# Kernel optimization log

Measured on AMD Instinct MI355X. Metric: run time of the kernel, lower is better.

Reference implementation:

```python
import math
import jax, jax.numpy as jnp
import numpy as np

GROUPS = 8

def setup_inputs() -> dict:
    key = jax.random.key(0)
    ks = jax.random.split(key, 6)
    N, H, W, C = 8, 128, 128, 512
    s = 1.0 / math.sqrt(C)
    return {
        "x": jax.random.normal(ks[0], (N, H, W, C), dtype=jnp.float32),
        "Wq": jax.random.normal(ks[1], (C, C), dtype=jnp.float32) * s,
        "Wk": jax.random.normal(ks[2], (C, C), dtype=jnp.float32) * s,
        "Wv": jax.random.normal(ks[3], (C, C), dtype=jnp.float32) * s,
        "Wo": jax.random.normal(ks[4], (C, C), dtype=jnp.float32) * s,
        "bo": jnp.zeros((C,), dtype=jnp.float32),
    }

def reference(x, Wq, Wk, Wv, Wo, bo):
    # width=False: attend along H axis -> permute to [N, W, H, C]
    x = jnp.transpose(x, (0, 2, 1, 3))
    N, W, H, C = x.shape
    g = GROUPS
    gp = C // g  # group_planes (head dim)
    xr = x.reshape(N * W, H, C)
    # torch nn.Linear: y = x @ W^T
    q = (xr @ Wq.T).reshape(N * W, H, g, gp)
    k = (xr @ Wk.T).reshape(N * W, H, g, gp)
    v = (xr @ Wv.T).reshape(N * W, H, g, gp)
    attn = jnp.einsum('nigc,njgc->nijg', q, k / math.sqrt(gp))
    attn = jax.nn.softmax(attn, axis=2)
    out = jnp.einsum('nijg,njgc->nigc', attn, v)
    out = out.reshape(N * W, H, C)
    out = out @ Wo.T + bo
    out = out.reshape(N, W, H, C)
    return jnp.transpose(out, (0, 2, 1, 3))
```

## Files before the change

kernel.cpp:

```cpp
#include <hip/hip_runtime.h>
#include <stdint.h>


typedef __attribute__((ext_vector_type(4))) float f32x4;
typedef __attribute__((ext_vector_type(8))) short bf16x8;
typedef unsigned short u16;
typedef unsigned int u32;

#define CBAR() asm volatile("" ::: "memory")
#define SBAR() do { CBAR(); __builtin_amdgcn_s_barrier(); CBAR(); } while(0)
#define LGKM0() do { asm volatile("s_waitcnt lgkmcnt(0)" ::: "memory"); __builtin_amdgcn_sched_barrier(0); } while(0)
#define VMC(n) asm volatile("s_waitcnt vmcnt(" #n ")" ::: "memory")

static __device__ __forceinline__ u16 f2bf(float f){
    union { float f; u32 u; } v; v.f = f;
    u32 r = v.u + 0x7fffu + ((v.u >> 16) & 1u);
    return (u16)(r >> 16);
}

static __device__ __forceinline__ void gload16(const void* g, void* l){
    __builtin_amdgcn_global_load_lds((const __attribute__((address_space(1))) void*)g,
                                     (__attribute__((address_space(3))) void*)l, 16, 0, 0);
}

__global__ void k_wconv(const float* __restrict__ Wq, const float* __restrict__ Wk,
                        const float* __restrict__ Wv, const float* __restrict__ Wo,
                        u16* __restrict__ Wcat, u16* __restrict__ Wob){
    int e = (blockIdx.x * 256 + threadIdx.x) * 4;
    if (e < 1536*512) {
        int row = e >> 9, col = e & 511;
        const float* s = (row < 512) ? (Wq + row*512)
                        : (row < 1024 ? Wk + (row-512)*512 : Wv + (row-1024)*512);
        float4 v = *(const float4*)(s + col);
        ushort4 o = { f2bf(v.x), f2bf(v.y), f2bf(v.z), f2bf(v.w) };
        *(ushort4*)(Wcat + e) = o;
    } else {
        int e2 = e - 1536*512;
        float4 v = *(const float4*)(Wo + e2);
        ushort4 o = { f2bf(v.x), f2bf(v.y), f2bf(v.z), f2bf(v.w) };
        *(ushort4*)(Wob + e2) = o;
    }
}

__global__ void k_xconv(const float* __restrict__ x, u16* __restrict__ xb, int n0){
    int t = blockIdx.x * 256 + threadIdx.x;
    int ml = t >> 6;
    int c0 = (t & 63) << 3;
    int nl = ml >> 7, h = ml & 127;
    int n = n0 + nl, nb = n >> 7, w = n & 127;
    const float* src = x + (size_t)((nb*128 + h)*128 + w) * 512 + c0;
    float4 a = *(const float4*)(src);
    float4 b = *(const float4*)(src + 4);
    uint4 o;
    o.x = (u32)f2bf(a.x) | ((u32)f2bf(a.y) << 16);
    o.y = (u32)f2bf(a.z) | ((u32)f2bf(a.w) << 16);
    o.z = (u32)f2bf(b.x) | ((u32)f2bf(b.y) << 16);
    o.w = (u32)f2bf(b.z) | ((u32)f2bf(b.w) << 16);
    *(uint4*)(xb + (size_t)ml*512 + c0) = o;
}

template<int NCOL, bool OUTPROJ>
__global__ __launch_bounds__(512, 2) void k_gemm4(const u16* __restrict__ A, const u16* __restrict__ B,
                                                  void* __restrict__ Cout, const float* __restrict__ bias,
                                                  int n0, int nrow, int planesz){
    extern __shared__ char smc[];
    const int tid = threadIdx.x;
    const int wid = tid >> 6, lane = tid & 63, lg = lane >> 4, li = lane & 15;
    const int wm = wid >> 2, wn = wid & 3;
    const int bid = blockIdx.x;
    const int xcd = bid & 7, l = bid >> 3;
    const int row_tile = xcd * (nrow >> 3) + l / NCOL;
    const int col_tile = l % NCOL;
    const int m0 = row_tile * 256, nn0 = col_tile * 256;

    auto stageA = [&](int st){
        char* sl = smc + (st & 3)*32768;
        const int kb = st*32;
        #pragma unroll
        for (int i = 0; i < 2; ++i) {
            int R = wid*32 + i*16;
            int r = R + (lane >> 2);
            int cq = (lane & 3) ^ ((r >> 1) & 3);
            gload16((const char*)(A + (size_t)(m0 + r)*512 + kb) + cq*16, sl + R*64);
        }
    };
    auto stageB = [&](int st){
        char* sl = smc + (st & 3)*32768 + 16384;
        const int kb = st*32;
        #pragma unroll
        for (int i = 0; i < 2; ++i) {
            int R = wid*32 + i*16;
            int r = R + (lane >> 2);
            int cq = (lane & 3) ^ ((r >> 1) & 3);
            gload16((const char*)(B + (size_t)(nn0 + r)*512 + kb) + cq*16, sl + R*64);
        }
    };

    f32x4 acc[8][4];
    #pragma unroll
    for (int i = 0; i < 8; ++i)
        #pragma unroll
        for (int j = 0; j < 4; ++j)
            acc[i][j] = f32x4{0.f, 0.f, 0.f, 0.f};

    stageA(0); stageB(0);
    stageA(1); stageB(1);
    stageA(2); stageB(2);
    VMC(8);
    SBAR();

    bf16x8 af[4], bfr[4];
    for (int t = 0; t < 16; ++t) {
        char* sl = smc + (t & 3)*32768;

        #pragma unroll
        for (int f = 0; f < 4; ++f) {
            int ra = wm*128 + f*16 + li;
            af[f] = *(const bf16x8*)(sl + ra*64 + (((lg ^ (ra >> 1)) & 3) << 4));
        }
        #pragma unroll
        for (int f = 0; f < 4; ++f) {
            int rb = wn*64 + f*16 + li;
            bfr[f] = *(const bf16x8*)(sl + 16384 + rb*64 + (((lg ^ (rb >> 1)) & 3) << 4));
        }
        if (t < 13) stageA(t + 3);
        SBAR(); LGKM0();
        __builtin_amdgcn_s_setprio(1);
        #pragma unroll
        for (int fi = 0; fi < 4; ++fi)
            #pragma unroll
            for (int fj = 0; fj < 4; ++fj)
                acc[fi][fj] = __builtin_amdgcn_mfma_f32_16x16x32_bf16(af[fi], bfr[fj], acc[fi][fj], 0, 0, 0);
        __builtin_amdgcn_s_setprio(0);
        SBAR();

        #pragma unroll
        for (int f = 0; f < 4; ++f) {
            int ra = wm*128 + (4 + f)*16 + li;
            af[f] = *(const bf16x8*)(sl + ra*64 + (((lg ^ (ra >> 1)) & 3) << 4));
        }
        if (t < 13) stageB(t + 3);
        SBAR(); LGKM0();
        __builtin_amdgcn_s_setprio(1);
        #pragma unroll
        for (int fi = 0; fi < 4; ++fi)
            #pragma unroll
            for (int fj = 0; fj < 4; ++fj)
                acc[4 + fi][fj] = __builtin_amdgcn_mfma_f32_16x16x32_bf16(af[fi], bfr[fj], acc[4 + fi][fj], 0, 0, 0);
        __builtin_amdgcn_s_setprio(0);
        if (t < 13)      { VMC(8); }
        else if (t == 13){ VMC(4); }
        else if (t == 14){ VMC(0); }
        SBAR();
    }

    if (!OUTPROJ) {
        u16* Cp = (u16*)Cout + (size_t)(nn0 >> 9) * planesz;
        const int cb = (nn0 & 511) + wn*64;
        #pragma unroll
        for (int mf = 0; mf < 8; ++mf)
            #pragma unroll
            for (int nf = 0; nf < 4; ++nf)
                #pragma unroll
                for (int r = 0; r < 4; ++r) {
                    int row = m0 + wm*128 + mf*16 + lg*4 + r;
                    int col = cb + nf*16 + li;
                    Cp[(size_t)row*512 + col] = f2bf(acc[mf][nf][r]);
                }
    } else {
        float* C = (float*)Cout;
        #pragma unroll
        for (int mf = 0; mf < 8; ++mf)
            #pragma unroll
            for (int nf = 0; nf < 4; ++nf)
                #pragma unroll
                for (int r = 0; r < 4; ++r) {
                    int row = m0 + wm*128 + mf*16 + lg*4 + r;
                    int col = nn0 + wn*64 + nf*16 + li;
                    int mg = n0*128 + row;
                    int n = mg >> 7, ii = mg & 127;
                    int nb = n >> 7, w = n & 127;
                    C[(size_t)((nb*128 + ii)*128 + w) * 512 + col] = acc[mf][nf][r] + bias[col];
                }
    }
}

__global__ __launch_bounds__(256, 2) void k_attn(const u16* __restrict__ Qpl, const u16* __restrict__ Kpl,
                                                 const u16* __restrict__ Vpl, u16* __restrict__ Ob){
    __shared__ char sm[52224];
    const int g = blockIdx.x;
    const int nl = blockIdx.y;
    const int tid = threadIdx.x;
    const int wid = tid >> 6, lane = tid & 63, lg = lane >> 4, li = lane & 15;

    const u16* Qg = Qpl + (size_t)nl*128*512 + g*64;
    const u16* Kg = Kpl + (size_t)nl*128*512 + g*64;
    const u16* Vg = Vpl + (size_t)nl*128*512 + g*64;
    u16*       Og = Ob  + (size_t)nl*128*512 + g*64;

    #pragma unroll
    for (int it = 0; it < 4; ++it) {
        int gi = it*256 + tid;
        int row = gi >> 3, gs = gi & 7;
        int sw = (gs ^ (row & 7)) << 4;
        gload16((const char*)(Qg + (size_t)row*512) + sw, sm + it*4096 + wid*1024);
        gload16((const char*)(Kg + (size_t)row*512) + sw, sm + 16384 + it*4096 + wid*1024);
    }
    {
        int j = tid & 127, ch = tid >> 7;
        const u16* src = Vg + (size_t)j*512 + ch*32;
        uint4 a0 = *(const uint4*)(src);
        uint4 a1 = *(const uint4*)(src + 8);
        uint4 a2 = *(const uint4*)(src + 16);
        uint4 a3 = *(const uint4*)(src + 24);
        u32 w[16] = {a0.x,a0.y,a0.z,a0.w, a1.x,a1.y,a1.z,a1.w,
                     a2.x,a2.y,a2.z,a2.w, a3.x,a3.y,a3.z,a3.w};
        char* dst = sm + 34816 + ch*32*272 + j*2;
        #pragma unroll
        for (int cc = 0; cc < 32; ++cc) {
            u32 word = w[cc >> 1];
            u16 val = (cc & 1) ? (u16)(word >> 16) : (u16)(word & 0xffffu);
            *(u16*)(dst + cc*272) = val;
        }
    }
    __syncthreads();

    const int i0w = wid*32;
    f32x4 s[2][8];
    #pragma unroll
    for (int t = 0; t < 2; ++t)
        #pragma unroll
        for (int tj = 0; tj < 8; ++tj)
            s[t][tj] = f32x4{0.f,0.f,0.f,0.f};

    #pragma unroll
    for (int ks = 0; ks < 2; ++ks) {
        bf16x8 qf[2];
        #pragma unroll
        for (int t = 0; t < 2; ++t) {
            int ra = i0w + t*16 + li;
            qf[t] = *(const bf16x8*)(sm + ra*128 + ((ks*64 + lg*16) ^ ((ra & 7) << 4)));
        }
        #pragma unroll
        for (int tj = 0; tj < 8; ++tj) {
            int rb = tj*16 + li;
            bf16x8 kf = *(const bf16x8*)(sm + 16384 + rb*128 + ((ks*64 + lg*16) ^ ((rb & 7) << 4)));
            #pragma unroll
            for (int t = 0; t < 2; ++t)
                s[t][tj] = __builtin_amdgcn_mfma_f32_16x16x32_bf16(qf[t], kf, s[t][tj], 0, 0, 0);
        }
    }
    __syncthreads();

    char* pb = sm + wid*8704;
    #pragma unroll
    for (int t = 0; t < 2; ++t) {
        #pragma unroll
        for (int r = 0; r < 4; ++r) {
            float mx = -1e30f;
            #pragma unroll
            for (int tj = 0; tj < 8; ++tj) mx = fmaxf(mx, s[t][tj][r]);
            #pragma unroll
            for (int off = 1; off < 16; off <<= 1) mx = fmaxf(mx, __shfl_xor(mx, off, 64));
            float p[8]; float sum = 0.f;
            #pragma unroll
            for (int tj = 0; tj < 8; ++tj) { p[tj] = __expf((s[t][tj][r] - mx)*0.125f); sum += p[tj]; }
            #pragma unroll
            for (int off = 1; off < 16; off <<= 1) sum += __shfl_xor(sum, off, 64);
            float inv = 1.0f / sum;
            int prow = t*16 + lg*4 + r;
            #pragma unroll
            for (int tj = 0; tj < 8; ++tj)
                *(u16*)(pb + prow*272 + (tj*16 + li)*2) = f2bf(p[tj]*inv);
        }
    }

    f32x4 o[2][4];
    #pragma unroll
    for (int t = 0; t < 2; ++t)
        #pragma unroll
        for (int tc = 0; tc < 4; ++tc)
            o[t][tc] = f32x4{0.f,0.f,0.f,0.f};

    #pragma unroll
    for (int ks = 0; ks < 4; ++ks) {
        bf16x8 pf[2];
        #pragma unroll
        for (int t = 0; t < 2; ++t)
            pf[t] = *(const bf16x8*)(pb + (t*16 + li)*272 + (ks*64 + lg*16));
        #pragma unroll
        for (int tc = 0; tc < 4; ++tc) {
            bf16x8 vf = *(const bf16x8*)(sm + 34816 + (tc*16 + li)*272 + (ks*64 + lg*16));
            #pragma unroll
            for (int t = 0; t < 2; ++t)
                o[t][tc] = __builtin_amdgcn_mfma_f32_16x16x32_bf16(pf[t], vf, o[t][tc], 0, 0, 0);
        }
    }

    #pragma unroll
    for (int t = 0; t < 2; ++t)
        #pragma unroll
        for (int tc = 0; tc < 4; ++tc)
            #pragma unroll
            for (int r = 0; r < 4; ++r) {
                int irow = i0w + t*16 + lg*4 + r;
                int col = tc*16 + li;
                Og[(size_t)irow*512 + col] = f2bf(o[t][tc][r]);
            }
}

extern "C" void kernel_launch(void* const* d_in, const int* in_sizes, int n_in,
                              void* d_out, int out_size, void* d_ws, size_t ws_size,
                              hipStream_t stream){
    const float* x  = (const float*)d_in[0];
    const float* Wq = (const float*)d_in[1];
    const float* Wk = (const float*)d_in[2];
    const float* Wv = (const float*)d_in[3];
    const float* Wo = (const float*)d_in[4];
    const float* bo = (const float*)d_in[5];

    char* ws = (char*)d_ws;
    u16* Wcat = (u16*)ws;
    u16* Wob  = Wcat + 1536*512;

    int CN = 1024;
    while (CN > 64 && (size_t)2097152 + (size_t)CN*524288 > ws_size) CN >>= 1;
    u16* xb   = (u16*)(ws + 2097152);
    u16* QKV2 = xb + (size_t)CN*128*512;
    int planesz = CN*128*512;

    hipFuncSetAttribute((const void*)&k_gemm4<6, false>,
                        hipFuncAttributeMaxDynamicSharedMemorySize, 131072);
    hipFuncSetAttribute((const void*)&k_gemm4<2, true>,
                        hipFuncAttributeMaxDynamicSharedMemorySize, 131072);

    k_wconv<<<1024, 256, 0, stream>>>(Wq, Wk, Wv, Wo, Wcat, Wob);
    int nch = 1024 / CN;
    for (int ch = 0; ch < nch; ++ch) {
        int n0 = ch * CN;
        int nrow = (CN * 128) / 256;
        k_xconv<<<CN*32, 256, 0, stream>>>(x, xb, n0);
        k_gemm4<6, false><<<nrow*6, 512, 131072, stream>>>(xb, Wcat, QKV2, nullptr, 0, nrow, planesz);
        k_attn<<<dim3(8, CN), 256, 0, stream>>>(QKV2, QKV2 + planesz, QKV2 + 2*(size_t)planesz, xb);
        k_gemm4<2, true ><<<nrow*2, 512, 131072, stream>>>(xb, Wob, d_out, bo, n0, nrow, 0);
    }
}
```

Measured before the change: 632.2 us.

## Remap out-projection tiles so each tile writes contiguous output rows

The out-projection GEMM now gathers A rows as a permuted set: each 256-row tile covers two h values across all 128 w positions. Its fp32 stores then form contiguous 128-row runs in the NHWC output instead of rows strided by 128*512 floats. The A and B load base addresses are precomputed once per thread rather than recomputed for every stage. The minimum chunk size rises to 128 so the tile mapping stays valid, at the cost of scattered A-row reads from the bf16 intermediate.

```diff
diff --git a/kernel.cpp b/kernel.cpp
--- a/kernel.cpp
+++ b/kernel.cpp
@@ -72,28 +72,32 @@
     const int row_tile = xcd * (nrow >> 3) + l / NCOL;
     const int col_tile = l % NCOL;
     const int m0 = row_tile * 256, nn0 = col_tile * 256;
-
+    const int nbL = row_tile >> 6, h0 = (row_tile & 63) * 2;
+
+    const char* baseA[2]; const char* baseB[2]; int dstR[2];
+    #pragma unroll
+    for (int i = 0; i < 2; ++i) {
+        int R = wid*32 + i*16;
+        int r = R + (lane >> 2);
+        int cq = (lane & 3) ^ ((r >> 1) & 3);
+        long arow;
+        if (OUTPROJ) arow = ((long)nbL*128 + (r & 127))*128 + h0 + (r >> 7);
+        else         arow = m0 + r;
+        baseA[i] = (const char*)(A + (size_t)arow*512) + cq*16;
+        baseB[i] = (const char*)(B + (size_t)(nn0 + r)*512) + cq*16;
+        dstR[i] = R;
+    }
     auto stageA = [&](int st){
         char* sl = smc + (st & 3)*32768;
-        const int kb = st*32;
-        #pragma unroll
-        for (int i = 0; i < 2; ++i) {
-            int R = wid*32 + i*16;
-            int r = R + (lane >> 2);
-            int cq = (lane & 3) ^ ((r >> 1) & 3);
-            gload16((const char*)(A + (size_t)(m0 + r)*512 + kb) + cq*16, sl + R*64);
-        }
+        #pragma unroll
+        for (int i = 0; i < 2; ++i)
+            gload16(baseA[i] + st*64, sl + dstR[i]*64);
     };
     auto stageB = [&](int st){
         char* sl = smc + (st & 3)*32768 + 16384;
-        const int kb = st*32;
-        #pragma unroll
-        for (int i = 0; i < 2; ++i) {
-            int R = wid*32 + i*16;
-            int r = R + (lane >> 2);
-            int cq = (lane & 3) ^ ((r >> 1) & 3);
-            gload16((const char*)(B + (size_t)(nn0 + r)*512 + kb) + cq*16, sl + R*64);
-        }
+        #pragma unroll
+        for (int i = 0; i < 2; ++i)
+            gload16(baseB[i] + st*64, sl + dstR[i]*64);
     };
 
     f32x4 acc[8][4];
@@ -169,18 +173,18 @@
                 }
     } else {
         float* C = (float*)Cout;
+        const int nbG = (n0 >> 7) + nbL;
         #pragma unroll
         for (int mf = 0; mf < 8; ++mf)
             #pragma unroll
             for (int nf = 0; nf < 4; ++nf)
                 #pragma unroll
                 for (int r = 0; r < 4; ++r) {
-                    int row = m0 + wm*128 + mf*16 + lg*4 + r;
+                    int rho = wm*128 + mf*16 + lg*4 + r;
+                    int w = rho & 127, hh = rho >> 7;
                     int col = nn0 + wn*64 + nf*16 + li;
-                    int mg = n0*128 + row;
-                    int n = mg >> 7, ii = mg & 127;
-                    int nb = n >> 7, w = n & 127;
-                    C[(size_t)((nb*128 + ii)*128 + w) * 512 + col] = acc[mf][nf][r] + bias[col];
+                    size_t orow = (size_t)(nbG*128 + h0 + hh)*128 + w;
+                    C[orow*512 + col] = acc[mf][nf][r] + bias[col];
                 }
     }
 }
@@ -324,7 +328,7 @@
     u16* Wob  = Wcat + 1536*512;
 
     int CN = 1024;
-    while (CN > 64 && (size_t)2097152 + (size_t)CN*524288 > ws_size) CN >>= 1;
+    while (CN > 128 && (size_t)2097152 + (size_t)CN*524288 > ws_size) CN >>= 1;
     u16* xb   = (u16*)(ws + 2097152);
     u16* QKV2 = xb + (size_t)CN*128*512;
     int planesz = CN*128*512;
```

After: 615.4 us. 2.7% less time.
